# Kernel tuning notes

Measured on AMD Instinct MI355X. Metric: run time of the kernel, lower is better.

The kernel has to match this reference:

```python
import jax, jax.numpy as jnp
import numpy as np

D_MODEL = 256
D_FF = 1024
N_HEADS = 4
D_K = D_MODEL // N_HEADS
RMS_EPS = 1e-5
B, T = 4, 2048


def setup_inputs() -> dict:
    key = jax.random.key(0)
    ks = jax.random.split(key, 12)
    s = 0.02
    inp = {
        "x": jax.random.normal(ks[0], (B, T, D_MODEL), dtype=jnp.float32),
        # causal lower-triangular mask (True = attend)
        "causal_mask": jnp.tril(jnp.ones((1, 1, T, T), dtype=bool)),
        "rms_attn_w": jnp.ones((D_MODEL,), jnp.float32),
        "wq": jax.random.normal(ks[1], (D_MODEL, D_MODEL), jnp.float32) * s,
        "wk": jax.random.normal(ks[2], (D_MODEL, D_MODEL), jnp.float32) * s,
        "wv": jax.random.normal(ks[3], (D_MODEL, D_MODEL), jnp.float32) * s,
        "wo": jax.random.normal(ks[4], (D_MODEL, D_MODEL), jnp.float32) * s,
        "rms_ffn_w": jnp.ones((D_MODEL,), jnp.float32),
        "w_gate": jax.random.normal(ks[5], (D_FF, D_MODEL), jnp.float32) * s,
        "w_up": jax.random.normal(ks[6], (D_FF, D_MODEL), jnp.float32) * s,
        "w_down": jax.random.normal(ks[7], (D_MODEL, D_FF), jnp.float32) * s,
    }
    return inp


def _rmsnorm(x, w):
    rms = jnp.sqrt(jnp.mean(x * x, axis=-1, keepdims=True) + RMS_EPS)
    return x / rms * w


def reference(x, causal_mask, rms_attn_w, wq, wk, wv, wo, rms_ffn_w, w_gate, w_up, w_down):
    b, t, c = x.shape
    h = _rmsnorm(x, rms_attn_w)
    # torch Linear: y = x @ W.T, W is [out, in]
    q = (h @ wq.T).reshape(b, t, N_HEADS, D_K).transpose(0, 2, 1, 3)  # [B,H,T,Dk]
    k = (h @ wk.T).reshape(b, t, N_HEADS, D_K).transpose(0, 2, 1, 3)
    v = (h @ wv.T).reshape(b, t, N_HEADS, D_K).transpose(0, 2, 1, 3)
    scores = jnp.einsum("bhqd,bhkd->bhqk", q, k) / jnp.sqrt(jnp.float32(D_K))
    scores = jnp.where(causal_mask[:, :, :t, :t], scores, jnp.float32(-jnp.inf))
    attn = jax.nn.softmax(scores, axis=-1)
    out = jnp.einsum("bhqk,bhkd->bhqd", attn, v).transpose(0, 2, 1, 3).reshape(b, t, c)
    x = x + out @ wo.T
    hf = _rmsnorm(x, rms_ffn_w)
    ffn = (jax.nn.silu(hf @ w_gate.T) * (hf @ w_up.T)) @ w_down.T
    return x + ffn
```

## Files before the change

kernel.cpp:

```cpp
#include <hip/hip_runtime.h>
#include <hip/hip_bf16.h>
#include <math.h>

#define TT 2048
typedef __bf16 bf16x8 __attribute__((ext_vector_type(8)));
typedef float f32x4 __attribute__((ext_vector_type(4)));
typedef __hip_bfloat16 bf16;

static __device__ __forceinline__ f32x4 mfma16(bf16x8 a, bf16x8 b, f32x4 c) {
  return __builtin_amdgcn_mfma_f32_16x16x32_bf16(a, b, c, 0, 0, 0);
}
static __device__ __forceinline__ bf16x8 ldb8(const bf16* p) {
  return *(const bf16x8*)p;
}
static __device__ __forceinline__ unsigned short bfbits(float f) {
  bf16 b = __float2bfloat16(f);
  return *(unsigned short*)&b;
}
static __device__ __forceinline__ void gll16(const bf16* g, bf16* l) {
  __builtin_amdgcn_global_load_lds(
      (const __attribute__((address_space(1))) unsigned int*)g,
      (__attribute__((address_space(3))) unsigned int*)l, 16, 0, 0);
}

__global__ void __launch_bounds__(256) prep_kernel(
    const float* __restrict__ wq, const float* __restrict__ wk,
    const float* __restrict__ wv, const float* __restrict__ wo,
    const float* __restrict__ wg, const float* __restrict__ wu,
    const float* __restrict__ wd,
    bf16* __restrict__ Wqkv, bf16* __restrict__ Wo,
    bf16* __restrict__ Wgu, bf16* __restrict__ Wd,
    const float* __restrict__ x, const float* __restrict__ rmsw,
    bf16* __restrict__ hb) {
  if (blockIdx.x < 4096) {
    int idx = blockIdx.x * 256 + threadIdx.x;
    if (idx < 196608) {
      int row = idx >> 8, col = idx & 255;
      const float* src = row < 256 ? wq : (row < 512 ? wk : wv);
      Wqkv[idx] = __float2bfloat16(src[(row & 255) * 256 + col]);
    } else if (idx < 262144) {
      int i = idx - 196608;
      Wo[i] = __float2bfloat16(wo[i]);
    } else if (idx < 786432) {
      int i = idx - 262144;
      int row = i >> 8, col = i & 255;
      int t = row >> 4, r = row & 15;
      int f = (t >> 1) * 16 + r;
      const float* src = (t & 1) ? wu : wg;
      Wgu[i] = __float2bfloat16(src[f * 256 + col]);
    } else {
      int i = idx - 786432;
      Wd[i] = __float2bfloat16(wd[i]);
    }
  } else {
    const int wv_ = threadIdx.x >> 6, lane = threadIdx.x & 63;
    const int token = (blockIdx.x - 4096) * 4 + wv_;
    const float4 xv = ((const float4*)x)[token * 64 + lane];
    float ss = xv.x * xv.x + xv.y * xv.y + xv.z * xv.z + xv.w * xv.w;
#pragma unroll
    for (int off = 1; off < 64; off <<= 1) ss += __shfl_xor(ss, off, 64);
    const float inv = rsqrtf(ss * (1.0f / 256.0f) + 1e-5f);
    const float4 w4 = ((const float4*)rmsw)[lane];
    union { unsigned short u[4]; uint2 v2; } pk;
    pk.u[0] = bfbits(xv.x * inv * w4.x);
    pk.u[1] = bfbits(xv.y * inv * w4.y);
    pk.u[2] = bfbits(xv.z * inv * w4.z);
    pk.u[3] = bfbits(xv.w * inv * w4.w);
    ((uint2*)hb)[token * 64 + lane] = pk.v2;
  }
}

__global__ void __launch_bounds__(256) rmsnorm_kernel(
    const float* __restrict__ x, const float* __restrict__ w, bf16* __restrict__ out) {
  const int wv = threadIdx.x >> 6, lane = threadIdx.x & 63;
  const int token = blockIdx.x * 4 + wv;
  const float4 xv = ((const float4*)x)[token * 64 + lane];
  float ss = xv.x * xv.x + xv.y * xv.y + xv.z * xv.z + xv.w * xv.w;
#pragma unroll
  for (int off = 1; off < 64; off <<= 1) ss += __shfl_xor(ss, off, 64);
  const float inv = rsqrtf(ss * (1.0f / 256.0f) + 1e-5f);
  const float4 w4 = ((const float4*)w)[lane];
  union { unsigned short u[4]; uint2 v2; } pk;
  pk.u[0] = bfbits(xv.x * inv * w4.x);
  pk.u[1] = bfbits(xv.y * inv * w4.y);
  pk.u[2] = bfbits(xv.z * inv * w4.z);
  pk.u[3] = bfbits(xv.w * inv * w4.w);
  ((uint2*)out)[token * 64 + lane] = pk.v2;
}

template <int BM, int BN, int KC>
static __device__ __forceinline__ void gemm_chunks(
    const bf16* __restrict__ Ag, const bf16* __restrict__ Bg,
    int lda, int ldb, int ktot,
    bf16* ldsA, bf16* ldsB, int wave, int lane,
    f32x4 (&acc)[BM / 32][BN / 32]) {
  const int lo = lane & 15, hi = lane >> 4;
  const int wm = (wave >> 1) * (BM / 2), wn = (wave & 1) * (BN / 2);
  const int lrow = lane >> 2, lcol = (lane & 3) * 8;
  for (int kc = 0; kc < ktot; kc += KC) {
    __syncthreads();
#pragma unroll
    for (int c = 0; c < KC / 32; c++) {
      for (int is = wave; is < BM / 16; is += 4)
        gll16(Ag + (size_t)(is * 16 + lrow) * lda + kc + c * 32 + lcol,
              ldsA + c * (BM * 32) + is * 512);
      for (int is = wave; is < BN / 16; is += 4)
        gll16(Bg + (size_t)(is * 16 + lrow) * ldb + kc + c * 32 + lcol,
              ldsB + c * (BN * 32) + is * 512);
    }
    __syncthreads();
#pragma unroll
    for (int c = 0; c < KC / 32; c++) {
      bf16x8 af[BM / 32], bfr[BN / 32];
#pragma unroll
      for (int i = 0; i < BM / 32; i++)
        af[i] = ldb8(ldsA + c * (BM * 32) + (wm + i * 16 + lo) * 32 + hi * 8);
#pragma unroll
      for (int j = 0; j < BN / 32; j++)
        bfr[j] = ldb8(ldsB + c * (BN * 32) + (wn + j * 16 + lo) * 32 + hi * 8);
#pragma unroll
      for (int i = 0; i < BM / 32; i++)
#pragma unroll
        for (int j = 0; j < BN / 32; j++)
          acc[i][j] = mfma16(bfr[j], af[i], acc[i][j]);
    }
  }
}

__global__ void __launch_bounds__(256) qkv_gemm(
    const bf16* __restrict__ A, const bf16* __restrict__ W,
    bf16* __restrict__ qb, bf16* __restrict__ kb, bf16* __restrict__ vtb) {
  __shared__ __align__(16) bf16 ldsA[128 * 128], ldsB[64 * 128];
  const int wave = threadIdx.x >> 6, lane = threadIdx.x & 63;
  const int lo = lane & 15, hi = lane >> 4;
  const int wm = (wave >> 1) * 64, wn = (wave & 1) * 32;
  f32x4 acc[4][2];
#pragma unroll
  for (int i = 0; i < 4; i++)
#pragma unroll
    for (int j = 0; j < 2; j++) acc[i][j] = (f32x4){0.f, 0.f, 0.f, 0.f};
  gemm_chunks<128, 64, 128>(A + (size_t)blockIdx.x * 128 * 256,
                            W + (size_t)blockIdx.y * 64 * 256,
                            256, 256, 256, ldsA, ldsB, wave, lane, acc);
#pragma unroll
  for (int i = 0; i < 4; i++) {
    const int m = blockIdx.x * 128 + wm + i * 16 + lo;
    const int b = m >> 11, t = m & (TT - 1);
#pragma unroll
    for (int j = 0; j < 2; j++) {
      const int o0 = blockIdx.y * 64 + wn + j * 16 + hi * 4;
      const int sel = o0 >> 8, hd = (o0 >> 6) & 3, d0 = o0 & 63;
      const int bh = b * 4 + hd;
      if (sel == 0) {
        union { unsigned short u[4]; uint2 v2; } pk;
#pragma unroll
        for (int r = 0; r < 4; r++) pk.u[r] = bfbits(acc[i][j][r] * 0.125f);
        *(uint2*)&qb[((size_t)bh * TT + t) * 64 + d0] = pk.v2;
      } else if (sel == 1) {
        union { unsigned short u[4]; uint2 v2; } pk;
#pragma unroll
        for (int r = 0; r < 4; r++) pk.u[r] = bfbits(acc[i][j][r]);
        *(uint2*)&kb[((size_t)bh * TT + t) * 64 + d0] = pk.v2;
      } else {
        bf16* vt = vtb + (size_t)bh * (64 * TT) + (t >> 5) * 2048 + (t & 31);
#pragma unroll
        for (int r = 0; r < 4; r++)
          vt[(d0 + r) * 32] = __float2bfloat16(acc[i][j][r]);
      }
    }
  }
}

__global__ void __launch_bounds__(256) attn_kernel(
    const bf16* __restrict__ qbp, const bf16* __restrict__ kbp,
    const bf16* __restrict__ vtp, bf16* __restrict__ aout) {
  const int wave = threadIdx.x >> 6, lane = threadIdx.x & 63;
  const int lo = lane & 15, hi = lane >> 4;
  const int bh = blockIdx.y;
  __shared__ __align__(16) unsigned short ldsP[4][2][16][40];
  __shared__ __align__(16) unsigned short ldsO[4][32][88];
  __shared__ float ldsL[4][2][16];
  const bf16* Q  = qbp + (size_t)bh * (TT * 64);
  const bf16* Kp = kbp + (size_t)bh * (TT * 64);
  const bf16* Vt = vtp + (size_t)bh * (64 * TT);
  const int b = bh >> 2, hd = bh & 3;

  for (int half = 0; half < 2; half++) {
    const int qt = half == 0 ? (int)blockIdx.x : 63 - (int)blockIdx.x;
    const int q0 = qt * 32;
    const int ns = qt + 1;
    bf16x8 aq[2][2];
#pragma unroll
    for (int mf = 0; mf < 2; mf++)
#pragma unroll
      for (int h = 0; h < 2; h++)
        aq[mf][h] = ldb8(Q + (q0 + mf * 16 + lo) * 64 + h * 32 + hi * 8);
    f32x4 acc[2][4];
#pragma unroll
    for (int mf = 0; mf < 2; mf++)
#pragma unroll
      for (int dt = 0; dt < 4; dt++) acc[mf][dt] = (f32x4){0.f, 0.f, 0.f, 0.f};
    float lsum[2] = {0.f, 0.f};

    int i = wave;
    bf16x8 kf[2][2];
    if (i < ns) {
#pragma unroll
      for (int ct = 0; ct < 2; ct++) {
        const bf16* kr = Kp + (i * 32 + ct * 16 + lo) * 64 + hi * 8;
        kf[ct][0] = ldb8(kr);
        kf[ct][1] = ldb8(kr + 32);
      }
    }
    for (; i < ns; i += 4) {
      const int kt0 = i * 32;
      f32x4 s[2][2];
#pragma unroll
      for (int mf = 0; mf < 2; mf++)
#pragma unroll
        for (int ct = 0; ct < 2; ct++) {
          f32x4 sc = (f32x4){0.f, 0.f, 0.f, 0.f};
          sc = mfma16(kf[ct][0], aq[mf][0], sc);
          sc = mfma16(kf[ct][1], aq[mf][1], sc);
          s[mf][ct] = sc;
        }
      const int ktn = (i + 4 < ns ? i + 4 : i) * 32;
      bf16x8 kn[2][2];
#pragma unroll
      for (int ct = 0; ct < 2; ct++) {
        const bf16* kr = Kp + (ktn + ct * 16 + lo) * 64 + hi * 8;
        kn[ct][0] = ldb8(kr);
        kn[ct][1] = ldb8(kr + 32);
      }
      const bf16* vtile = Vt + i * 2048;
      bf16x8 vb[4];
#pragma unroll
      for (int dt = 0; dt < 4; dt++)
        vb[dt] = ldb8(vtile + (dt * 16 + lo) * 32 + hi * 8);
      if (i == ns - 1) {
#pragma unroll
        for (int mf = 0; mf < 2; mf++)
#pragma unroll
          for (int ct = 0; ct < 2; ct++)
#pragma unroll
            for (int r = 0; r < 4; r++)
              if (kt0 + ct * 16 + hi * 4 + r > q0 + mf * 16 + lo) s[mf][ct][r] = -INFINITY;
      }
#pragma unroll
      for (int mf = 0; mf < 2; mf++)
#pragma unroll
        for (int ct = 0; ct < 2; ct++) {
          union { unsigned short u[4]; uint2 v2; } pk;
#pragma unroll
          for (int r = 0; r < 4; r++) {
            const float p = __expf(s[mf][ct][r]);
            lsum[mf] += p;
            pk.u[r] = bfbits(p);
          }
          *(uint2*)&ldsP[wave][mf][lo][ct * 16 + hi * 4] = pk.v2;
        }
      asm volatile("s_waitcnt lgkmcnt(0)" ::: "memory");
      bf16x8 pa[2];
#pragma unroll
      for (int mf = 0; mf < 2; mf++)
        pa[mf] = *(const bf16x8*)&ldsP[wave][mf][lo][hi * 8];
#pragma unroll
      for (int mf = 0; mf < 2; mf++)
#pragma unroll
        for (int dt = 0; dt < 4; dt++)
          acc[mf][dt] = mfma16(vb[dt], pa[mf], acc[mf][dt]);
#pragma unroll
      for (int ct = 0; ct < 2; ct++) {
        kf[ct][0] = kn[ct][0];
        kf[ct][1] = kn[ct][1];
      }
    }

#pragma unroll
    for (int mf = 0; mf < 2; mf++) {
      lsum[mf] += __shfl_xor(lsum[mf], 16, 64);
      lsum[mf] += __shfl_xor(lsum[mf], 32, 64);
    }
    if (hi == 0) {
      ldsL[wave][0][lo] = lsum[0];
      ldsL[wave][1][lo] = lsum[1];
    }
#pragma unroll
    for (int mf = 0; mf < 2; mf++)
#pragma unroll
      for (int dt = 0; dt < 4; dt++) {
        union { unsigned short u[4]; uint2 v2; } pk;
#pragma unroll
        for (int r = 0; r < 4; r++) pk.u[r] = bfbits(acc[mf][dt][r]);
        *(uint2*)&ldsO[wave][mf * 16 + lo][dt * 16 + hi * 4] = pk.v2;
      }
    __syncthreads();

    const int q = threadIdx.x >> 3;
    const int d0 = (threadIdx.x & 7) * 8;
    const float L = ldsL[0][q >> 4][q & 15] + ldsL[1][q >> 4][q & 15] +
                    ldsL[2][q >> 4][q & 15] + ldsL[3][q >> 4][q & 15];
    float o[8] = {0.f, 0.f, 0.f, 0.f, 0.f, 0.f, 0.f, 0.f};
#pragma unroll
    for (int w = 0; w < 4; w++) {
      const bf16x8 v = *(const bf16x8*)&ldsO[w][q][d0];
#pragma unroll
      for (int j = 0; j < 8; j++) o[j] += (float)v[j];
    }
    const float invL = 1.0f / L;
    bf16* dst = aout + ((size_t)(b * TT + q0 + q)) * 256 + hd * 64 + d0;
    union { unsigned short u[8]; uint4 v4; } pk;
#pragma unroll
    for (int j = 0; j < 8; j++) pk.u[j] = bfbits(o[j] * invL);
    *(uint4*)dst = pk.v4;
    __syncthreads();
  }
}

__global__ void __launch_bounds__(256) wo_gemm(
    const bf16* __restrict__ A, const bf16* __restrict__ W,
    const float* __restrict__ x, float* __restrict__ x2) {
  __shared__ __align__(16) bf16 ldsA[64 * 256], ldsB[64 * 256];
  const int wave = threadIdx.x >> 6, lane = threadIdx.x & 63;
  const int lo = lane & 15, hi = lane >> 4;
  const int wm = (wave >> 1) * 32, wn = (wave & 1) * 32;
  f32x4 acc[2][2];
#pragma unroll
  for (int i = 0; i < 2; i++)
#pragma unroll
    for (int j = 0; j < 2; j++) acc[i][j] = (f32x4){0.f, 0.f, 0.f, 0.f};
  gemm_chunks<64, 64, 256>(A + (size_t)blockIdx.x * 64 * 256,
                           W + (size_t)blockIdx.y * 64 * 256,
                           256, 256, 256, ldsA, ldsB, wave, lane, acc);
#pragma unroll
  for (int i = 0; i < 2; i++) {
    const int m = blockIdx.x * 64 + wm + i * 16 + lo;
#pragma unroll
    for (int j = 0; j < 2; j++) {
      const int col0 = blockIdx.y * 64 + wn + j * 16 + hi * 4;
      const size_t idx = (size_t)m * 256 + col0;
      const float4 xv = *(const float4*)&x[idx];
      float4 ov;
      ov.x = xv.x + acc[i][j][0];
      ov.y = xv.y + acc[i][j][1];
      ov.z = xv.z + acc[i][j][2];
      ov.w = xv.w + acc[i][j][3];
      *(float4*)&x2[idx] = ov;
    }
  }
}

__global__ void __launch_bounds__(256) gu_gemm(
    const bf16* __restrict__ A, const bf16* __restrict__ W, bf16* __restrict__ mid) {
  __shared__ __align__(16) bf16 ldsA[128 * 64], ldsB[128 * 64];
  const int wave = threadIdx.x >> 6, lane = threadIdx.x & 63;
  const int lo = lane & 15, hi = lane >> 4;
  const int wm = (wave >> 1) * 64, wn = (wave & 1) * 64;
  f32x4 acc[4][4];
#pragma unroll
  for (int i = 0; i < 4; i++)
#pragma unroll
    for (int j = 0; j < 4; j++) acc[i][j] = (f32x4){0.f, 0.f, 0.f, 0.f};
  gemm_chunks<128, 128, 64>(A + (size_t)blockIdx.x * 128 * 256,
                            W + (size_t)blockIdx.y * 128 * 256,
                            256, 256, 256, ldsA, ldsB, wave, lane, acc);
  const int B0 = blockIdx.y * 128 + wn;
#pragma unroll
  for (int i = 0; i < 4; i++) {
    const int m = blockIdx.x * 128 + wm + i * 16 + lo;
#pragma unroll
    for (int p = 0; p < 2; p++) {
      const int f0 = ((B0 >> 5) + p) * 16 + hi * 4;
      union { unsigned short u[4]; uint2 v2; } pk;
#pragma unroll
      for (int r = 0; r < 4; r++) {
        const float g = acc[i][2 * p][r];
        const float u = acc[i][2 * p + 1][r];
        pk.u[r] = bfbits(g / (1.f + __expf(-g)) * u);
      }
      *(uint2*)&mid[(size_t)m * 1024 + f0] = pk.v2;
    }
  }
}

__global__ void __launch_bounds__(256) down_gemm(
    const bf16* __restrict__ A, const bf16* __restrict__ W,
    const float* __restrict__ x2, float* __restrict__ out) {
  __shared__ __align__(16) bf16 ldsA[64 * 256], ldsB[64 * 256];
  const int wave = threadIdx.x >> 6, lane = threadIdx.x & 63;
  const int lo = lane & 15, hi = lane >> 4;
  const int wm = (wave >> 1) * 32, wn = (wave & 1) * 32;
  f32x4 acc[2][2];
#pragma unroll
  for (int i = 0; i < 2; i++)
#pragma unroll
    for (int j = 0; j < 2; j++) acc[i][j] = (f32x4){0.f, 0.f, 0.f, 0.f};
  gemm_chunks<64, 64, 256>(A + (size_t)blockIdx.x * 64 * 1024,
                           W + (size_t)blockIdx.y * 64 * 1024,
                           1024, 1024, 1024, ldsA, ldsB, wave, lane, acc);
#pragma unroll
  for (int i = 0; i < 2; i++) {
    const int m = blockIdx.x * 64 + wm + i * 16 + lo;
#pragma unroll
    for (int j = 0; j < 2; j++) {
      const int col0 = blockIdx.y * 64 + wn + j * 16 + hi * 4;
      const size_t idx = (size_t)m * 256 + col0;
      const float4 xv = *(const float4*)&x2[idx];
      float4 ov;
      ov.x = xv.x + acc[i][j][0];
      ov.y = xv.y + acc[i][j][1];
      ov.z = xv.z + acc[i][j][2];
      ov.w = xv.w + acc[i][j][3];
      *(float4*)&out[idx] = ov;
    }
  }
}

extern "C" void kernel_launch(void* const* d_in, const int* in_sizes, int n_in,
                              void* d_out, int out_size, void* d_ws, size_t ws_size,
                              hipStream_t stream) {
  const float* x          = (const float*)d_in[0];
  const float* rms_attn_w = (const float*)d_in[2];
  const float* wq         = (const float*)d_in[3];
  const float* wk         = (const float*)d_in[4];
  const float* wv         = (const float*)d_in[5];
  const float* wo         = (const float*)d_in[6];
  const float* rms_ffn_w  = (const float*)d_in[7];
  const float* wg         = (const float*)d_in[8];
  const float* wu         = (const float*)d_in[9];
  const float* wd         = (const float*)d_in[10];
  float* out = (float*)d_out;
  char* ws = (char*)d_ws;

  bf16* Wqkv  = (bf16*)(ws + 0);
  bf16* Wo    = (bf16*)(ws + 393216);
  bf16* Wgu   = (bf16*)(ws + 524288);
  bf16* Wd    = (bf16*)(ws + 1572864);
  bf16* hb    = (bf16*)(ws + 2097152);
  bf16* qb    = (bf16*)(ws + 6291456);
  bf16* kb    = (bf16*)(ws + 10485760);
  bf16* vtb   = (bf16*)(ws + 14680064);
  bf16* attnb = (bf16*)(ws + 18874368);
  float* x2   = (float*)(ws + 23068672);
  bf16* h2b   = (bf16*)(ws + 31457280);
  bf16* midb  = (bf16*)(ws + 35651584);

  hipLaunchKernelGGL(prep_kernel, dim3(6144), dim3(256), 0, stream,
                     wq, wk, wv, wo, wg, wu, wd, Wqkv, Wo, Wgu, Wd,
                     x, rms_attn_w, hb);
  hipLaunchKernelGGL(qkv_gemm, dim3(64, 12), dim3(256), 0, stream, hb, Wqkv, qb, kb, vtb);
  hipLaunchKernelGGL(attn_kernel, dim3(32, 16), dim3(256), 0, stream, qb, kb, vtb, attnb);
  hipLaunchKernelGGL(wo_gemm, dim3(128, 4), dim3(256), 0, stream, attnb, Wo, x, x2);
  hipLaunchKernelGGL(rmsnorm_kernel, dim3(2048), dim3(256), 0, stream, x2, rms_ffn_w, h2b);
  hipLaunchKernelGGL(gu_gemm, dim3(64, 16), dim3(256), 0, stream, h2b, Wgu, midb);
  hipLaunchKernelGGL(down_gemm, dim3(128, 4), dim3(256), 0, stream, midb, Wd, x2, out);
}
```

Measured before the change: 164.3 us.

## Fuse FFN RMSNorm into Wo GEMM epilogue and prefetch V tiles in attention

```diff
diff --git a/kernel.cpp b/kernel.cpp
--- a/kernel.cpp
+++ b/kernel.cpp
@@ -70,24 +70,6 @@
   }
 }
 
-__global__ void __launch_bounds__(256) rmsnorm_kernel(
-    const float* __restrict__ x, const float* __restrict__ w, bf16* __restrict__ out) {
-  const int wv = threadIdx.x >> 6, lane = threadIdx.x & 63;
-  const int token = blockIdx.x * 4 + wv;
-  const float4 xv = ((const float4*)x)[token * 64 + lane];
-  float ss = xv.x * xv.x + xv.y * xv.y + xv.z * xv.z + xv.w * xv.w;
-#pragma unroll
-  for (int off = 1; off < 64; off <<= 1) ss += __shfl_xor(ss, off, 64);
-  const float inv = rsqrtf(ss * (1.0f / 256.0f) + 1e-5f);
-  const float4 w4 = ((const float4*)w)[lane];
-  union { unsigned short u[4]; uint2 v2; } pk;
-  pk.u[0] = bfbits(xv.x * inv * w4.x);
-  pk.u[1] = bfbits(xv.y * inv * w4.y);
-  pk.u[2] = bfbits(xv.z * inv * w4.z);
-  pk.u[3] = bfbits(xv.w * inv * w4.w);
-  ((uint2*)out)[token * 64 + lane] = pk.v2;
-}
-
 template <int BM, int BN, int KC>
 static __device__ __forceinline__ void gemm_chunks(
     const bf16* __restrict__ Ag, const bf16* __restrict__ Bg,
@@ -203,7 +185,7 @@
     float lsum[2] = {0.f, 0.f};
 
     int i = wave;
-    bf16x8 kf[2][2];
+    bf16x8 kf[2][2], vf[4];
     if (i < ns) {
 #pragma unroll
       for (int ct = 0; ct < 2; ct++) {
@@ -211,6 +193,10 @@
         kf[ct][0] = ldb8(kr);
         kf[ct][1] = ldb8(kr + 32);
       }
+      const bf16* vtile = Vt + i * 2048;
+#pragma unroll
+      for (int dt = 0; dt < 4; dt++)
+        vf[dt] = ldb8(vtile + (dt * 16 + lo) * 32 + hi * 8);
     }
     for (; i < ns; i += 4) {
       const int kt0 = i * 32;
@@ -224,19 +210,20 @@
           sc = mfma16(kf[ct][1], aq[mf][1], sc);
           s[mf][ct] = sc;
         }
-      const int ktn = (i + 4 < ns ? i + 4 : i) * 32;
-      bf16x8 kn[2][2];
+      const int in_ = (i + 4 < ns ? i + 4 : i);
+      bf16x8 kn[2][2], vn[4];
 #pragma unroll
       for (int ct = 0; ct < 2; ct++) {
-        const bf16* kr = Kp + (ktn + ct * 16 + lo) * 64 + hi * 8;
+        const bf16* kr = Kp + (in_ * 32 + ct * 16 + lo) * 64 + hi * 8;
         kn[ct][0] = ldb8(kr);
         kn[ct][1] = ldb8(kr + 32);
       }
-      const bf16* vtile = Vt + i * 2048;
-      bf16x8 vb[4];
-#pragma unroll
-      for (int dt = 0; dt < 4; dt++)
-        vb[dt] = ldb8(vtile + (dt * 16 + lo) * 32 + hi * 8);
+      {
+        const bf16* vtile = Vt + in_ * 2048;
+#pragma unroll
+        for (int dt = 0; dt < 4; dt++)
+          vn[dt] = ldb8(vtile + (dt * 16 + lo) * 32 + hi * 8);
+      }
       if (i == ns - 1) {
 #pragma unroll
         for (int mf = 0; mf < 2; mf++)
@@ -268,12 +255,14 @@
       for (int mf = 0; mf < 2; mf++)
 #pragma unroll
         for (int dt = 0; dt < 4; dt++)
-          acc[mf][dt] = mfma16(vb[dt], pa[mf], acc[mf][dt]);
+          acc[mf][dt] = mfma16(vf[dt], pa[mf], acc[mf][dt]);
 #pragma unroll
       for (int ct = 0; ct < 2; ct++) {
         kf[ct][0] = kn[ct][0];
         kf[ct][1] = kn[ct][1];
       }
+#pragma unroll
+      for (int dt = 0; dt < 4; dt++) vf[dt] = vn[dt];
     }
 
 #pragma unroll
@@ -317,36 +306,52 @@
   }
 }
 
-__global__ void __launch_bounds__(256) wo_gemm(
+__global__ void __launch_bounds__(256) wo_rms_gemm(
     const bf16* __restrict__ A, const bf16* __restrict__ W,
-    const float* __restrict__ x, float* __restrict__ x2) {
-  __shared__ __align__(16) bf16 ldsA[64 * 256], ldsB[64 * 256];
+    const float* __restrict__ x, float* __restrict__ x2,
+    const float* __restrict__ rmsw, bf16* __restrict__ h2b) {
+  __shared__ __align__(16) bf16 ldsA[32 * 64], ldsB[256 * 64];
+  __shared__ float ldsS[4][16];
   const int wave = threadIdx.x >> 6, lane = threadIdx.x & 63;
   const int lo = lane & 15, hi = lane >> 4;
-  const int wm = (wave >> 1) * 32, wn = (wave & 1) * 32;
-  f32x4 acc[2][2];
-#pragma unroll
-  for (int i = 0; i < 2; i++)
-#pragma unroll
-    for (int j = 0; j < 2; j++) acc[i][j] = (f32x4){0.f, 0.f, 0.f, 0.f};
-  gemm_chunks<64, 64, 256>(A + (size_t)blockIdx.x * 64 * 256,
-                           W + (size_t)blockIdx.y * 64 * 256,
+  const int wm = (wave >> 1) * 16, wn = (wave & 1) * 128;
+  f32x4 acc[1][8];
+#pragma unroll
+  for (int j = 0; j < 8; j++) acc[0][j] = (f32x4){0.f, 0.f, 0.f, 0.f};
+  gemm_chunks<32, 256, 64>(A + (size_t)blockIdx.x * 32 * 256, W,
                            256, 256, 256, ldsA, ldsB, wave, lane, acc);
-#pragma unroll
-  for (int i = 0; i < 2; i++) {
-    const int m = blockIdx.x * 64 + wm + i * 16 + lo;
-#pragma unroll
-    for (int j = 0; j < 2; j++) {
-      const int col0 = blockIdx.y * 64 + wn + j * 16 + hi * 4;
-      const size_t idx = (size_t)m * 256 + col0;
-      const float4 xv = *(const float4*)&x[idx];
-      float4 ov;
-      ov.x = xv.x + acc[i][j][0];
-      ov.y = xv.y + acc[i][j][1];
-      ov.z = xv.z + acc[i][j][2];
-      ov.w = xv.w + acc[i][j][3];
-      *(float4*)&x2[idx] = ov;
-    }
+  const int m = blockIdx.x * 32 + wm + lo;
+  float ss = 0.f;
+  float4 xv[8];
+#pragma unroll
+  for (int j = 0; j < 8; j++) {
+    const int col0 = wn + j * 16 + hi * 4;
+    const size_t idx = (size_t)m * 256 + col0;
+    float4 v = *(const float4*)&x[idx];
+    v.x += acc[0][j][0];
+    v.y += acc[0][j][1];
+    v.z += acc[0][j][2];
+    v.w += acc[0][j][3];
+    xv[j] = v;
+    *(float4*)&x2[idx] = v;
+    ss += v.x * v.x + v.y * v.y + v.z * v.z + v.w * v.w;
+  }
+  ss += __shfl_xor(ss, 16, 64);
+  ss += __shfl_xor(ss, 32, 64);
+  if (hi == 0) ldsS[wave][lo] = ss;
+  __syncthreads();
+  const float tot = ldsS[wave & 2][lo] + ldsS[(wave & 2) | 1][lo];
+  const float inv = rsqrtf(tot * (1.0f / 256.0f) + 1e-5f);
+#pragma unroll
+  for (int j = 0; j < 8; j++) {
+    const int col0 = wn + j * 16 + hi * 4;
+    const float4 w4 = *(const float4*)&rmsw[col0];
+    union { unsigned short u[4]; uint2 v2; } pk;
+    pk.u[0] = bfbits(xv[j].x * inv * w4.x);
+    pk.u[1] = bfbits(xv[j].y * inv * w4.y);
+    pk.u[2] = bfbits(xv[j].z * inv * w4.z);
+    pk.u[3] = bfbits(xv[j].w * inv * w4.w);
+    *(uint2*)&h2b[(size_t)m * 256 + col0] = pk.v2;
   }
 }
 
@@ -450,8 +455,8 @@
                      x, rms_attn_w, hb);
   hipLaunchKernelGGL(qkv_gemm, dim3(64, 12), dim3(256), 0, stream, hb, Wqkv, qb, kb, vtb);
   hipLaunchKernelGGL(attn_kernel, dim3(32, 16), dim3(256), 0, stream, qb, kb, vtb, attnb);
-  hipLaunchKernelGGL(wo_gemm, dim3(128, 4), dim3(256), 0, stream, attnb, Wo, x, x2);
-  hipLaunchKernelGGL(rmsnorm_kernel, dim3(2048), dim3(256), 0, stream, x2, rms_ffn_w, h2b);
+  hipLaunchKernelGGL(wo_rms_gemm, dim3(256), dim3(256), 0, stream,
+                     attnb, Wo, x, x2, rms_ffn_w, h2b);
   hipLaunchKernelGGL(gu_gemm, dim3(64, 16), dim3(256), 0, stream, h2b, Wgu, midb);
   hipLaunchKernelGGL(down_gemm, dim3(128, 4), dim3(256), 0, stream, midb, Wd, x2, out);
 }
```

New measurement: 166.8 us. Within noise of the previous version (+1.5%).
